# Performance work log

Hardware: AMD Instinct MI355X
Metric: run time of the kernel (lower is better)

## Reference

```python
import jax, jax.numpy as jnp
import numpy as np

# dims: L = 1 + H*W tokens (cls first), BT = B*T clips*frames
L, BT, D = 577, 128, 768
B, T = 16, 8
H = W = 24
CM = 192   # d_middle = D // REDUCTION(4)
CR = 48    # CM // rf_r(4)
K = 3      # rf_k and spatial kernel


def setup_inputs() -> dict:
    key = jax.random.key(0)
    ks = jax.random.split(key, 10)
    return {
        "x":      jax.random.normal(ks[0], (L, BT, D), jnp.float32),
        # tada_pre_proj: Linear(D -> CM)
        "w_pre":  jax.random.normal(ks[1], (D, CM), jnp.float32) * 0.02,
        "b_pre":  jnp.zeros((CM,), jnp.float32),
        # TAdaConv2dV2 base depthwise weight (1x3x3, groups=CM) and bias
        "w_base": jax.random.normal(ks[2], (K, K, 1, CM), jnp.float32) * 0.1,
        "b_conv": jnp.zeros((CM,), jnp.float32),
        # route function: global 1x1 branch, temporal conv a (CM->CR), temporal conv b (CR->CM, small init)
        "w_g":    jax.random.normal(ks[3], (CM, CM), jnp.float32) * 0.02,
        "b_g":    jnp.zeros((CM,), jnp.float32),
        "w_a":    jax.random.normal(ks[4], (K, CM, CR), jnp.float32) * 0.05,
        "b_a":    jnp.zeros((CR,), jnp.float32),
        "w_b":    jax.random.normal(ks[5], (K, CR, CM), jnp.float32) * 0.02,
        # tada_proj: Linear(CM -> D)
        "w_proj": jax.random.normal(ks[6], (CM, D), jnp.float32) * 0.02,
        "b_proj": jnp.zeros((D,), jnp.float32),
    }


def reference(x, w_pre, b_pre, w_base, b_conv, w_g, b_g, w_a, b_a, w_b, w_proj, b_proj):
    # --- tada_pre_proj ---
    h = x @ w_pre + b_pre                                   # [L, BT, CM]
    cls_tok, sp = h[:1], h[1:]                              # cls token bypasses the conv
    sp = sp.transpose(1, 0, 2).reshape(BT, H, W, CM)        # [BT, H, W, CM]

    # --- route function: per-frame, per-channel calibration alpha ---
    d = sp.reshape(B, T, H * W, CM).mean(axis=2)            # spatial avg pool -> [B, T, CM]
    g = d.mean(axis=1) @ w_g + b_g                          # global temporal descriptor [B, CM]
    a = jax.lax.conv_general_dilated(d + g[:, None, :], w_a, (1,), 'SAME',
                                     dimension_numbers=('NWC', 'WIO', 'NWC')) + b_a
    a = jax.nn.relu(a)                                      # [B, T, CR]
    alpha = jax.lax.conv_general_dilated(a, w_b, (1,), 'SAME',
                                         dimension_numbers=('NWC', 'WIO', 'NWC')) + 1.0  # [B, T, CM]

    # --- calibrated depthwise conv (cal_dim='cout') ---
    # conv2d(x, alpha * W_base) == alpha * conv2d(x, W_base) for depthwise cout calibration
    y = jax.lax.conv_general_dilated(sp, w_base, (1, 1), 'SAME',
                                     dimension_numbers=('NHWC', 'HWIO', 'NHWC'),
                                     feature_group_count=CM)
    y = y * alpha.reshape(BT, 1, 1, CM) + b_conv            # [BT, H, W, CM]
    y = y.reshape(BT, H * W, CM).transpose(1, 0, 2)         # [HW, BT, CM]
    out = jnp.concatenate([cls_tok, y], axis=0)             # [L, BT, CM]

    # --- QuickGELU + tada_proj ---
    out = out * jax.nn.sigmoid(1.702 * out)
    return out @ w_proj + b_proj                            # [L, BT, D]
```

## Files before the change

### kernel.cpp

```cpp
#include <hip/hip_runtime.h>

#define DEV __device__ __forceinline__

typedef short bf16x8 __attribute__((ext_vector_type(8)));
typedef float f32x4  __attribute__((ext_vector_type(4)));
typedef unsigned short ushort_t;


DEV unsigned short f2bf(float f) {
  unsigned u = __float_as_uint(f);
  unsigned r = (u + 0x7fffu + ((u >> 16) & 1u)) >> 16;
  return (unsigned short)r;
}

DEV unsigned cvt_pk_bf16(float a, float b) {
  unsigned r;
  asm("v_cvt_pk_bf16_f32 %0, %1, %2" : "=v"(r) : "v"(a), "v"(b));
  return r;
}

DEV float bf2f(unsigned short b) { return __uint_as_float((unsigned)b << 16); }

DEV float silu_g(float v) { return v / (1.f + __expf(-1.702f * v)); }

DEV void gload_lds16(const void* g, void* l) {
  __builtin_amdgcn_global_load_lds(
      (const __attribute__((address_space(1))) unsigned int*)g,
      (__attribute__((address_space(3))) unsigned int*)l, 16, 0, 0);
}

__global__ __launch_bounds__(256)
void prep_kernel(const float* __restrict__ w_pre, const float* __restrict__ w_proj,
                 short* __restrict__ w_preT, short* __restrict__ w_projT) {
  int i = blockIdx.x * 256 + threadIdx.x;
  if (i < 192 * 768) {
    int n = i / 768, k = i - n * 768;
    w_preT[i] = (short)f2bf(w_pre[k * 192 + n]);
    int n2 = i / 192, k2 = i - n2 * 192;
    w_projT[i] = (short)f2bf(w_proj[k2 * 768 + n2]);
  }
}

__global__ __launch_bounds__(512, 4)
void gemm1_kernel(const float* __restrict__ Af, const short* __restrict__ Bt,
                  const float* __restrict__ bias, ushort_t* __restrict__ C) {
  constexpr int BM = 128, BK = 64, KTOT = 768, NTOT = 192, NT = 12;
  __shared__ short As[2][BM * BK];
  __shared__ short Bs[2][192 * BK];

  const int tid  = threadIdx.x;
  const int wave = tid >> 6, lane = tid & 63;
  const int m0 = blockIdx.x * BM;
  const int wm = wave >> 2, wn = wave & 3;
  const int lr  = lane & 15;
  const int lk8 = lane >> 4;
  const int srow = lane >> 3;
  const int schunk = lane & 7;

  f32x4 acc[4][3] = {};
  float4 areg[2][2];

  auto loadA_f32 = [&](int kt) {
    #pragma unroll
    for (int s = 0; s < 2; ++s) {
      int id = tid + s * 512;
      int r = id >> 3, c = id & 7;
      int cg = c ^ (r & 7);
      const float* p = Af + (size_t)(m0 + r) * KTOT + kt + cg * 8;
      areg[s][0] = *(const float4*)p;
      areg[s][1] = *(const float4*)(p + 4);
    }
  };
  auto cvtStoreA = [&](int buf) {
    #pragma unroll
    for (int s = 0; s < 2; ++s) {
      int id = tid + s * 512;
      int r = id >> 3, c = id & 7;
      int4 w;
      w.x = (int)cvt_pk_bf16(areg[s][0].x, areg[s][0].y);
      w.y = (int)cvt_pk_bf16(areg[s][0].z, areg[s][0].w);
      w.z = (int)cvt_pk_bf16(areg[s][1].x, areg[s][1].y);
      w.w = (int)cvt_pk_bf16(areg[s][1].z, areg[s][1].w);
      *(int4*)&As[buf][r * 64 + c * 8] = w;
    }
  };
  auto stageB = [&](int kt, int buf) {
    #pragma unroll
    for (int j = 0; j < 3; ++j) {
      int rb8 = wave * 3 + j;
      int r = rb8 * 8 + srow;
      const short* src = Bt + (size_t)r * KTOT + kt + (schunk ^ srow) * 8;
      gload_lds16(src, (char*)Bs[buf] + rb8 * 1024);
    }
  };
  auto compute = [&](int buf) {
    #pragma unroll
    for (int ks = 0; ks < 2; ++ks) {
      int kc = ks * 4 + lk8;
      bf16x8 af[4], bfv[3];
      #pragma unroll
      for (int fm = 0; fm < 4; ++fm) {
        int row = wm * 64 + fm * 16 + lr;
        af[fm] = *(const bf16x8*)&As[buf][row * 64 + (kc ^ (row & 7)) * 8];
      }
      #pragma unroll
      for (int fn = 0; fn < 3; ++fn) {
        int row = wn * 48 + fn * 16 + lr;
        bfv[fn] = *(const bf16x8*)&Bs[buf][row * 64 + (kc ^ (row & 7)) * 8];
      }
      #pragma unroll
      for (int fm = 0; fm < 4; ++fm)
        #pragma unroll
        for (int fn = 0; fn < 3; ++fn)
          acc[fm][fn] = __builtin_amdgcn_mfma_f32_16x16x32_bf16(
              bfv[fn], af[fm], acc[fm][fn], 0, 0, 0);
    }
  };

  loadA_f32(0);
  cvtStoreA(0);
  stageB(0, 0);
  loadA_f32(BK);
  asm volatile("s_waitcnt vmcnt(4) lgkmcnt(0)" ::: "memory");
  __builtin_amdgcn_s_barrier();

  #pragma unroll
  for (int t = 0; t < NT; ++t) {
    const int cur = t & 1, nxt = cur ^ 1;
    if (t + 1 < NT) {
      stageB((t + 1) * BK, nxt);
      cvtStoreA(nxt);
      if (t + 2 < NT) loadA_f32((t + 2) * BK);
    }
    compute(cur);
    if (t + 1 < NT) {
      if (t + 2 < NT)
        asm volatile("s_waitcnt vmcnt(4) lgkmcnt(0)" ::: "memory");
      else
        asm volatile("s_waitcnt vmcnt(0) lgkmcnt(0)" ::: "memory");
      __builtin_amdgcn_s_barrier();
    }
  }

  const int cb = (lane >> 4) * 4;
  #pragma unroll
  for (int fm = 0; fm < 4; ++fm) {
    int row = m0 + wm * 64 + fm * 16 + lr;
    #pragma unroll
    for (int fn = 0; fn < 3; ++fn) {
      int col = wn * 48 + fn * 16 + cb;
      float4 bv = *(const float4*)(bias + col);
      int2 w;
      w.x = (int)cvt_pk_bf16(acc[fm][fn][0] + bv.x, acc[fm][fn][1] + bv.y);
      w.y = (int)cvt_pk_bf16(acc[fm][fn][2] + bv.z, acc[fm][fn][3] + bv.w);
      *(int2*)&C[(size_t)row * NTOT + col] = w;
    }
  }
}

__global__ __launch_bounds__(384)
void reduce_d_kernel(const ushort_t* __restrict__ h, float* __restrict__ d) {
  const int bt = blockIdx.x, tid = threadIdx.x;
  const int slice = tid / 24, c8 = tid % 24;
  __shared__ float part[16][192];
  float sum[8] = {};
  #pragma unroll 4
  for (int i = 0; i < 36; ++i) {
    int l = 1 + slice * 36 + i;
    bf16x8 v = *(const bf16x8*)&h[((size_t)l * 128 + bt) * 192 + c8 * 8];
    #pragma unroll
    for (int j = 0; j < 8; ++j) sum[j] += bf2f((unsigned short)v[j]);
  }
  #pragma unroll
  for (int j = 0; j < 8; ++j) part[slice][c8 * 8 + j] = sum[j];
  __syncthreads();
  if (tid < 192) {
    float s = 0.f;
    #pragma unroll
    for (int sl = 0; sl < 16; ++sl) s += part[sl][tid];
    d[bt * 192 + tid] = s * (1.f / 576.f);
  }
}

__global__ __launch_bounds__(256)
void small_path_kernel(const float* __restrict__ d,
                       const float* __restrict__ w_g, const float* __restrict__ b_g,
                       const float* __restrict__ w_a, const float* __restrict__ b_a,
                       const float* __restrict__ w_b,
                       float* __restrict__ alpha) {
  const int b = blockIdx.x, tid = threadIdx.x;
  __shared__ unsigned short wg_buf[36864];
  __shared__ unsigned short wa_buf[27648];
  __shared__ float e[8][192];
  __shared__ float md[192];
  __shared__ float a[8][48];

  #pragma unroll
  for (int it = 0; it < 36; ++it) {
    int i = tid + it * 256;
    float4 v = *(const float4*)(w_g + i * 4);
    int2 w;
    w.x = (int)cvt_pk_bf16(v.x, v.y);
    w.y = (int)cvt_pk_bf16(v.z, v.w);
    *(int2*)&wg_buf[i * 4] = w;
  }
  #pragma unroll
  for (int it = 0; it < 27; ++it) {
    int i = tid + it * 256;
    float4 v = *(const float4*)(w_a + i * 4);
    int2 w;
    w.x = (int)cvt_pk_bf16(v.x, v.y);
    w.y = (int)cvt_pk_bf16(v.z, v.w);
    *(int2*)&wa_buf[i * 4] = w;
  }
  for (int i = tid; i < 384; i += 256)
    *(float4*)((float*)e + i * 4) = *(const float4*)(d + (size_t)b * 1536 + i * 4);
  __syncthreads();

  if (tid < 192) {
    float m = 0.f;
    #pragma unroll
    for (int t = 0; t < 8; ++t) m += e[t][tid];
    md[tid] = m * 0.125f;
  }
  __syncthreads();

  if (tid < 192) {
    float accg = b_g[tid];
    #pragma unroll 8
    for (int k = 0; k < 192; ++k)
      accg += md[k] * bf2f(wg_buf[k * 192 + tid]);
    #pragma unroll
    for (int t = 0; t < 8; ++t) e[t][tid] += accg;
  }
  __syncthreads();

  #pragma unroll
  for (int it = 0; it < 27; ++it) {
    int i = tid + it * 256;
    float4 v = *(const float4*)(w_b + i * 4);
    int2 w;
    w.x = (int)cvt_pk_bf16(v.x, v.y);
    w.y = (int)cvt_pk_bf16(v.z, v.w);
    *(int2*)&wg_buf[i * 4] = w;
  }
  for (int o = tid; o < 384; o += 256) {
    int t = o / 48, r = o - t * 48;
    float acc = b_a[r];
    #pragma unroll
    for (int dt = 0; dt < 3; ++dt) {
      int tt = t + dt - 1;
      if ((unsigned)tt < 8u) {
        #pragma unroll 8
        for (int k = 0; k < 192; ++k)
          acc += e[tt][k] * bf2f(wa_buf[(dt * 192 + k) * 48 + r]);
      }
    }
    a[t][r] = fmaxf(acc, 0.f);
  }
  __syncthreads();

  if (tid < 192) {
    #pragma unroll
    for (int t = 0; t < 8; ++t) {
      float acc = 1.0f;
      #pragma unroll
      for (int dt = 0; dt < 3; ++dt) {
        int tt = t + dt - 1;
        if ((unsigned)tt < 8u) {
          #pragma unroll 8
          for (int r = 0; r < 48; ++r)
            acc += a[tt][r] * bf2f(wg_buf[(dt * 48 + r) * 192 + tid]);
        }
      }
      alpha[(size_t)(b * 8 + t) * 192 + tid] = acc;
    }
  }
}

__global__ __launch_bounds__(512, 3)
void fused_out_kernel(const ushort_t* __restrict__ h, const float* __restrict__ alpha,
                      const float* __restrict__ w_base, const float* __restrict__ b_conv,
                      const short* __restrict__ Bt, const float* __restrict__ bias,
                      float* __restrict__ out) {
  constexpr int NTOT = 768;
  __shared__ ushort_t Stile[64 * 192];

  const int tid  = threadIdx.x;
  const int bidx = blockIdx.x;
  const int q = 1154 >> 3, r = 1154 & 7;
  const int xcd = bidx & 7, pos = bidx >> 3;
  const int logical = (xcd < r) ? xcd * (q + 1) + pos
                                : r * (q + 1) + (xcd - r) * q + pos;
  const int l    = logical >> 1;
  const int bt0  = (logical & 1) * 64;
  const int wave = tid >> 6, lane = tid & 63;
  const int wm = wave >> 2, wn = wave & 3;
  const int lr = lane & 15, lk8 = lane >> 4;

  const int row = tid >> 3;
  const int cg  = tid & 7;
  const int bt  = bt0 + row;
  if (l == 0) {
    #pragma unroll
    for (int j = 0; j < 3; ++j) {
      int c8 = cg + 8 * j;
      bf16x8 hv = *(const bf16x8*)&h[(size_t)bt * 192 + c8 * 8];
      float v0 = silu_g(bf2f((ushort_t)hv[0])), v1 = silu_g(bf2f((ushort_t)hv[1]));
      float v2 = silu_g(bf2f((ushort_t)hv[2])), v3 = silu_g(bf2f((ushort_t)hv[3]));
      float v4 = silu_g(bf2f((ushort_t)hv[4])), v5 = silu_g(bf2f((ushort_t)hv[5]));
      float v6 = silu_g(bf2f((ushort_t)hv[6])), v7 = silu_g(bf2f((ushort_t)hv[7]));
      int4 pk;
      pk.x = (int)cvt_pk_bf16(v0, v1); pk.y = (int)cvt_pk_bf16(v2, v3);
      pk.z = (int)cvt_pk_bf16(v4, v5); pk.w = (int)cvt_pk_bf16(v6, v7);
      int chp = (c8 & ~7) | ((c8 & 7) ^ (row & 7));
      *(int4*)&Stile[row * 192 + chp * 8] = pk;
    }
  } else {
    const int p = l - 1, hh = p / 24, ww = p - hh * 24;
    const bool interior = (hh > 0) & (hh < 23) & (ww > 0) & (ww < 23);
    if (interior) {
      #pragma unroll
      for (int j = 0; j < 3; ++j) {
        int c8 = cg + 8 * j;
        int cbase = c8 * 8;
        bf16x8 hv[9];
        #pragma unroll
        for (int dh = 0; dh < 3; ++dh)
          #pragma unroll
          for (int dw = 0; dw < 3; ++dw)
            hv[dh * 3 + dw] = *(const bf16x8*)
                &h[((size_t)(1 + (hh + dh - 1) * 24 + (ww + dw - 1)) * 128 + bt) * 192 + cbase];
        float acc8[8] = {};
        #pragma unroll
        for (int t9 = 0; t9 < 9; ++t9) {
          const float* wp = w_base + t9 * 192 + cbase;
          float4 w0 = *(const float4*)wp, w1 = *(const float4*)(wp + 4);
          acc8[0] += bf2f((ushort_t)hv[t9][0]) * w0.x;
          acc8[1] += bf2f((ushort_t)hv[t9][1]) * w0.y;
          acc8[2] += bf2f((ushort_t)hv[t9][2]) * w0.z;
          acc8[3] += bf2f((ushort_t)hv[t9][3]) * w0.w;
          acc8[4] += bf2f((ushort_t)hv[t9][4]) * w1.x;
          acc8[5] += bf2f((ushort_t)hv[t9][5]) * w1.y;
          acc8[6] += bf2f((ushort_t)hv[t9][6]) * w1.z;
          acc8[7] += bf2f((ushort_t)hv[t9][7]) * w1.w;
        }
        const float* ap = alpha + (size_t)bt * 192 + cbase;
        float4 a0 = *(const float4*)ap, a1 = *(const float4*)(ap + 4);
        const float* bp = b_conv + cbase;
        float4 c0 = *(const float4*)bp, c1 = *(const float4*)(bp + 4);
        float v0 = silu_g(acc8[0] * a0.x + c0.x), v1 = silu_g(acc8[1] * a0.y + c0.y);
        float v2 = silu_g(acc8[2] * a0.z + c0.z), v3 = silu_g(acc8[3] * a0.w + c0.w);
        float v4 = silu_g(acc8[4] * a1.x + c1.x), v5 = silu_g(acc8[5] * a1.y + c1.y);
        float v6 = silu_g(acc8[6] * a1.z + c1.z), v7 = silu_g(acc8[7] * a1.w + c1.w);
        int4 pk;
        pk.x = (int)cvt_pk_bf16(v0, v1); pk.y = (int)cvt_pk_bf16(v2, v3);
        pk.z = (int)cvt_pk_bf16(v4, v5); pk.w = (int)cvt_pk_bf16(v6, v7);
        int chp = (c8 & ~7) | ((c8 & 7) ^ (row & 7));
        *(int4*)&Stile[row * 192 + chp * 8] = pk;
      }
    } else {
      #pragma unroll
      for (int j = 0; j < 3; ++j) {
        int c8 = cg + 8 * j;
        int cbase = c8 * 8;
        float acc8[8] = {};
        #pragma unroll
        for (int dh = 0; dh < 3; ++dh) {
          int y = hh + dh - 1;
          if ((unsigned)y >= 24u) continue;
          #pragma unroll
          for (int dw = 0; dw < 3; ++dw) {
            int xx = ww + dw - 1;
            if ((unsigned)xx >= 24u) continue;
            bf16x8 hv = *(const bf16x8*)
                &h[((size_t)(1 + y * 24 + xx) * 128 + bt) * 192 + cbase];
            const float* wp = w_base + (dh * 3 + dw) * 192 + cbase;
            float4 w0 = *(const float4*)wp, w1 = *(const float4*)(wp + 4);
            acc8[0] += bf2f((ushort_t)hv[0]) * w0.x;
            acc8[1] += bf2f((ushort_t)hv[1]) * w0.y;
            acc8[2] += bf2f((ushort_t)hv[2]) * w0.z;
            acc8[3] += bf2f((ushort_t)hv[3]) * w0.w;
            acc8[4] += bf2f((ushort_t)hv[4]) * w1.x;
            acc8[5] += bf2f((ushort_t)hv[5]) * w1.y;
            acc8[6] += bf2f((ushort_t)hv[6]) * w1.z;
            acc8[7] += bf2f((ushort_t)hv[7]) * w1.w;
          }
        }
        const float* ap = alpha + (size_t)bt * 192 + cbase;
        float4 a0 = *(const float4*)ap, a1 = *(const float4*)(ap + 4);
        const float* bp = b_conv + cbase;
        float4 c0 = *(const float4*)bp, c1 = *(const float4*)(bp + 4);
        float v0 = silu_g(acc8[0] * a0.x + c0.x), v1 = silu_g(acc8[1] * a0.y + c0.y);
        float v2 = silu_g(acc8[2] * a0.z + c0.z), v3 = silu_g(acc8[3] * a0.w + c0.w);
        float v4 = silu_g(acc8[4] * a1.x + c1.x), v5 = silu_g(acc8[5] * a1.y + c1.y);
        float v6 = silu_g(acc8[6] * a1.z + c1.z), v7 = silu_g(acc8[7] * a1.w + c1.w);
        int4 pk;
        pk.x = (int)cvt_pk_bf16(v0, v1); pk.y = (int)cvt_pk_bf16(v2, v3);
        pk.z = (int)cvt_pk_bf16(v4, v5); pk.w = (int)cvt_pk_bf16(v6, v7);
        int chp = (c8 & ~7) | ((c8 & 7) ^ (row & 7));
        *(int4*)&Stile[row * 192 + chp * 8] = pk;
      }
    }
  }
  __syncthreads();

  const int cb = (lane >> 4) * 4;
  #pragma unroll 1
  for (int nc = 0; nc < 4; ++nc) {
    const int n0 = nc * 192;
    bf16x8 bfv[6][3];
    #pragma unroll
    for (int kt = 0; kt < 6; ++kt)
      #pragma unroll
      for (int fn = 0; fn < 3; ++fn)
        bfv[kt][fn] = *(const bf16x8*)(Bt +
            (size_t)(n0 + wn * 48 + fn * 16 + lr) * 192 + kt * 32 + lk8 * 8);

    f32x4 acc[2][3] = {};
    #pragma unroll
    for (int kt = 0; kt < 6; ++kt) {
      bf16x8 af[2];
      #pragma unroll
      for (int fm = 0; fm < 2; ++fm) {
        int sr = wm * 32 + fm * 16 + lr;
        int kc = kt * 4 + lk8;
        int chp = (kc & ~7) | ((kc & 7) ^ (sr & 7));
        af[fm] = *(const bf16x8*)&Stile[sr * 192 + chp * 8];
      }
      #pragma unroll
      for (int fm = 0; fm < 2; ++fm)
        #pragma unroll
        for (int fn = 0; fn < 3; ++fn)
          acc[fm][fn] = __builtin_amdgcn_mfma_f32_16x16x32_bf16(
              bfv[kt][fn], af[fm], acc[fm][fn], 0, 0, 0);
    }

    #pragma unroll
    for (int fm = 0; fm < 2; ++fm) {
      int orow = l * 128 + bt0 + wm * 32 + fm * 16 + lr;
      #pragma unroll
      for (int fn = 0; fn < 3; ++fn) {
        int col = n0 + wn * 48 + fn * 16 + cb;
        float4 bv = *(const float4*)(bias + col);
        f32x4 o;
        o[0] = acc[fm][fn][0] + bv.x;
        o[1] = acc[fm][fn][1] + bv.y;
        o[2] = acc[fm][fn][2] + bv.z;
        o[3] = acc[fm][fn][3] + bv.w;
        __builtin_nontemporal_store(o, (f32x4*)&out[(size_t)orow * NTOT + col]);
      }
    }
  }
}

extern "C" void kernel_launch(void* const* d_in, const int* in_sizes, int n_in,
                              void* d_out, int out_size, void* d_ws, size_t ws_size,
                              hipStream_t stream) {
  (void)in_sizes; (void)n_in; (void)out_size; (void)ws_size;
  const float* x      = (const float*)d_in[0];
  const float* w_pre  = (const float*)d_in[1];
  const float* b_pre  = (const float*)d_in[2];
  const float* w_base = (const float*)d_in[3];
  const float* b_conv = (const float*)d_in[4];
  const float* w_g    = (const float*)d_in[5];
  const float* b_g    = (const float*)d_in[6];
  const float* w_a    = (const float*)d_in[7];
  const float* b_a    = (const float*)d_in[8];
  const float* w_b    = (const float*)d_in[9];
  const float* w_proj = (const float*)d_in[10];
  const float* b_proj = (const float*)d_in[11];

  float* out = (float*)d_out;
  char* ws = (char*)d_ws;
  short* w_preT  = (short*)(ws);
  short* w_projT = (short*)(ws + 294912);
  float* dbuf    = (float*)(ws + 589824);
  float* alpha   = (float*)(ws + 688128);
  ushort_t* h    = (ushort_t*)(ws + 786432);

  prep_kernel<<<576, 256, 0, stream>>>(w_pre, w_proj, w_preT, w_projT);

  gemm1_kernel<<<577, 512, 0, stream>>>(x, w_preT, b_pre, h);

  reduce_d_kernel<<<128, 384, 0, stream>>>(h, dbuf);
  small_path_kernel<<<16, 256, 0, stream>>>(dbuf, w_g, b_g, w_a, b_a, w_b, alpha);

  fused_out_kernel<<<1154, 512, 0, stream>>>(h, alpha, w_base, b_conv,
                                             w_projT, b_proj, out);
}
```

Measured before the change: 239.2 us.

## Double-buffer projection weight loads with inline asm and explicit vmcnt waits

The output-projection loop is rewritten as a software pipeline over eight half-chunks. Weight fragments are loaded with inline-asm global loads into two alternating register buffers, and explicit s_waitcnt vmcnt counts with sched barriers let the next half's loads overlap the current half's MFMAs. Before, each of the four N-chunks loaded all of its B fragments and only then computed. The wait counts must account for the interleaved nontemporal stores and bias loads; a miscount would give wrong results, and the extra buffers raise register pressure.

After: 246.0 us. 2.9% more time.

```diff
diff --git a/kernel.cpp b/kernel.cpp
--- a/kernel.cpp
+++ b/kernel.cpp
@@ -4,6 +4,7 @@
 
 typedef short bf16x8 __attribute__((ext_vector_type(8)));
 typedef float f32x4  __attribute__((ext_vector_type(4)));
+typedef int   i32x4  __attribute__((ext_vector_type(4)));
 typedef unsigned short ushort_t;
 
 
@@ -277,6 +278,11 @@
     }
   }
 }
+
+#define WAIT_SB(N) do { \
+    asm volatile("s_waitcnt vmcnt(" #N ")" ::: "memory"); \
+    __builtin_amdgcn_sched_barrier(0); \
+  } while (0)
 
 __global__ __launch_bounds__(512, 3)
 void fused_out_kernel(const ushort_t* __restrict__ h, const float* __restrict__ alpha,
@@ -406,25 +412,34 @@
   __syncthreads();
 
   const int cb = (lane >> 4) * 4;
-  #pragma unroll 1
-  for (int nc = 0; nc < 4; ++nc) {
-    const int n0 = nc * 192;
-    bf16x8 bfv[6][3];
-    #pragma unroll
-    for (int kt = 0; kt < 6; ++kt)
-      #pragma unroll
-      for (int fn = 0; fn < 3; ++fn)
-        bfv[kt][fn] = *(const bf16x8*)(Bt +
-            (size_t)(n0 + wn * 48 + fn * 16 + lr) * 192 + kt * 32 + lk8 * 8);
-
-    f32x4 acc[2][3] = {};
-    #pragma unroll
-    for (int kt = 0; kt < 6; ++kt) {
+  i32x4 bA[9], bB[9];
+
+  auto issue_half = [&](int hh2, i32x4* dst) {
+    const int nc = hh2 >> 1, k0 = (hh2 & 1) * 3;
+    #pragma unroll
+    for (int fn = 0; fn < 3; ++fn) {
+      const short* base = Bt + (size_t)(nc * 192 + wn * 48 + fn * 16 + lr) * 192
+                          + k0 * 32 + lk8 * 8;
+      asm volatile("global_load_dwordx4 %0, %1, off"
+                   : "=&v"(dst[fn * 3 + 0]) : "v"(base));
+      asm volatile("global_load_dwordx4 %0, %1, off offset:64"
+                   : "=&v"(dst[fn * 3 + 1]) : "v"(base));
+      asm volatile("global_load_dwordx4 %0, %1, off offset:128"
+                   : "=&v"(dst[fn * 3 + 2]) : "v"(base));
+    }
+  };
+
+  f32x4 acc[2][3];
+
+  auto mfma_half = [&](int hh2, i32x4* cur) {
+    const int k0 = (hh2 & 1) * 3;
+    #pragma unroll
+    for (int kk = 0; kk < 3; ++kk) {
+      const int kc = (k0 + kk) * 4 + lk8;
       bf16x8 af[2];
       #pragma unroll
       for (int fm = 0; fm < 2; ++fm) {
         int sr = wm * 32 + fm * 16 + lr;
-        int kc = kt * 4 + lk8;
         int chp = (kc & ~7) | ((kc & 7) ^ (sr & 7));
         af[fm] = *(const bf16x8*)&Stile[sr * 192 + chp * 8];
       }
@@ -433,9 +448,21 @@
         #pragma unroll
         for (int fn = 0; fn < 3; ++fn)
           acc[fm][fn] = __builtin_amdgcn_mfma_f32_16x16x32_bf16(
-              bfv[kt][fn], af[fm], acc[fm][fn], 0, 0, 0);
-    }
-
+              __builtin_bit_cast(bf16x8, cur[fn * 3 + kk]), af[fm],
+              acc[fm][fn], 0, 0, 0);
+    }
+  };
+
+  auto zero_acc = [&]() {
+    #pragma unroll
+    for (int fm = 0; fm < 2; ++fm)
+      #pragma unroll
+      for (int fn = 0; fn < 3; ++fn)
+        acc[fm][fn] = (f32x4){0.f, 0.f, 0.f, 0.f};
+  };
+
+  auto store_chunk = [&](int nc) {
+    const int n0 = nc * 192;
     #pragma unroll
     for (int fm = 0; fm < 2; ++fm) {
       int orow = l * 128 + bt0 + wm * 32 + fm * 16 + lr;
@@ -444,14 +471,26 @@
         int col = n0 + wn * 48 + fn * 16 + cb;
         float4 bv = *(const float4*)(bias + col);
         f32x4 o;
-        o[0] = acc[fm][fn][0] + bv.x;
-        o[1] = acc[fm][fn][1] + bv.y;
-        o[2] = acc[fm][fn][2] + bv.z;
-        o[3] = acc[fm][fn][3] + bv.w;
+        o[0] = acc[fm][fn][0] + bv.x; o[1] = acc[fm][fn][1] + bv.y;
+        o[2] = acc[fm][fn][2] + bv.z; o[3] = acc[fm][fn][3] + bv.w;
         __builtin_nontemporal_store(o, (f32x4*)&out[(size_t)orow * NTOT + col]);
       }
     }
-  }
+  };
+
+  issue_half(0, bA);
+  zero_acc();
+  issue_half(1, bB); WAIT_SB(9);  mfma_half(0, bA);
+  issue_half(2, bA); WAIT_SB(9);  mfma_half(1, bB); store_chunk(0);
+  zero_acc();
+  issue_half(3, bB); WAIT_SB(15); mfma_half(2, bA);
+  issue_half(4, bA); WAIT_SB(9);  mfma_half(3, bB); store_chunk(1);
+  zero_acc();
+  issue_half(5, bB); WAIT_SB(15); mfma_half(4, bA);
+  issue_half(6, bA); WAIT_SB(9);  mfma_half(5, bB); store_chunk(2);
+  zero_acc();
+  issue_half(7, bB); WAIT_SB(15); mfma_half(6, bA);
+  WAIT_SB(0);                     mfma_half(7, bB); store_chunk(3);
 }
 
 extern "C" void kernel_launch(void* const* d_in, const int* in_sizes, int n_in,
```
